# Optimization experiments

Hardware: AMD Instinct MI355X
Metric: run time of the kernel (lower is better)

The kernel has to match this reference:

```python
import jax, jax.numpy as jnp
import numpy as np

N_HEADS = 16
D_MODEL = 1024
D_K = D_MODEL // N_HEADS


def setup_inputs() -> dict:
    key = jax.random.key(0)
    ks = jax.random.split(key, 7)
    B, S = 2, 2048
    init = 0.02
    return {
        "query": jax.random.normal(ks[0], (B, S, D_MODEL), dtype=jnp.float32),
        "key": jax.random.normal(ks[1], (B, S, D_MODEL), dtype=jnp.float32),
        "value": jax.random.normal(ks[2], (B, S, D_MODEL), dtype=jnp.float32),
        "W_q": jax.random.normal(ks[3], (D_MODEL, D_MODEL), dtype=jnp.float32) * init,
        "W_k": jax.random.normal(ks[4], (D_MODEL, D_MODEL), dtype=jnp.float32) * init,
        "W_v": jax.random.normal(ks[5], (D_MODEL, D_MODEL), dtype=jnp.float32) * init,
        "W_o": jax.random.normal(ks[6], (D_MODEL, D_MODEL), dtype=jnp.float32) * init,
    }


def _split_heads(x):
    # (B, S, d_model) -> (B, H, S, d_k)
    B, S, _ = x.shape
    return x.reshape(B, S, N_HEADS, D_K).transpose(0, 2, 1, 3)


def reference(query, key, value, W_q, W_k, W_v, W_o):
    scale = jnp.sqrt(jnp.asarray(D_K, dtype=query.dtype))
    # torch Linear: y = x @ W.T
    Q = _split_heads(query @ W_q.T)   # (B,H,Sq,dk)
    K = _split_heads(key @ W_k.T)     # (B,H,Sk,dk)
    V = _split_heads(value @ W_v.T)   # (B,H,Sk,dk)
    scores = jnp.einsum("bhqd,bhkd->bhqk", Q, K) / scale
    attn = jax.nn.softmax(scores, axis=-1)           # (B,H,Sq,Sk); dropout p=0 -> identity
    attn_weights = attn.mean(axis=1)                 # (B,Sq,Sk) interpretable weights
    head_out = jnp.einsum("bhqk,bhkd->bqhd", attn, V)  # (B,Sq,H,dk)
    # NOTE: the original computes a head-gating (W_h) whose result is overwritten
    # by the concat below -> dead code, omitted.
    B, Sq = head_out.shape[0], head_out.shape[1]
    out = head_out.reshape(B, Sq, D_MODEL) @ W_o.T   # (B,Sq,d_model)
    return (out, attn_weights)
```

## Files before the change

### kernel.cpp

```cpp
#include <hip/hip_runtime.h>
#include <hip/hip_bf16.h>

#define Bq 2
#define Hh 16
#define Ss 2048
#define Dm 1024
#define Dk 64
#define SCALE 0.125f

typedef _Float16 f16x8 __attribute__((ext_vector_type(8)));
typedef _Float16 f16x4 __attribute__((ext_vector_type(4)));
typedef float    f32x4 __attribute__((ext_vector_type(4)));


__device__ __forceinline__ void gl_lds16(const void* g, void* lds) {
    __builtin_amdgcn_global_load_lds(
        (const __attribute__((address_space(1))) void*)g,
        (__attribute__((address_space(3))) void*)lds, 16, 0, 0);
}

__global__ __launch_bounds__(256) void convert_kernel(
    const float* __restrict__ q, const float* __restrict__ k,
    const float* __restrict__ v, const float* __restrict__ wq,
    const float* __restrict__ wk, const float* __restrict__ wv,
    const float* __restrict__ wo,
    _Float16* __restrict__ qd, _Float16* __restrict__ kd,
    _Float16* __restrict__ vd, _Float16* __restrict__ wd)
{
    int seg = blockIdx.y;
    const float* src; _Float16* dst; int n4;
    switch (seg) {
        case 0: src = q; dst = qd; n4 = 1048576; break;
        case 1: src = k; dst = kd; n4 = 1048576; break;
        case 2: src = v; dst = vd; n4 = 1048576; break;
        default:
            src = (seg == 3) ? wq : (seg == 4) ? wk : (seg == 5) ? wv : wo;
            dst = wd + (size_t)(seg - 3) * 1048576;
            n4 = 262144;
    }
    for (int i = blockIdx.x * 256 + threadIdx.x; i < n4; i += gridDim.x * 256) {
        float4 x = ((const float4*)src)[i];
        f16x4 h = {(_Float16)x.x, (_Float16)x.y, (_Float16)x.z, (_Float16)x.w};
        ((f16x4*)dst)[i] = h;
    }
}

__global__ __launch_bounds__(256) void gemm_qkv(
    const _Float16* __restrict__ qf, const _Float16* __restrict__ kf,
    const _Float16* __restrict__ vf, const _Float16* __restrict__ Wh,
    _Float16* __restrict__ Qd, _Float16* __restrict__ Kd,
    _Float16* __restrict__ Vd)
{
    __shared__ _Float16 As[128 * 32];
    __shared__ _Float16 Ws[128 * 32];
    int z = blockIdx.z;
    const _Float16* A = (z == 0) ? qf : (z == 1) ? kf : vf;
    const _Float16* W = Wh + (size_t)z * (Dm * Dm);
    int t = threadIdx.x, lane = t & 63, w = t >> 6;
    int quad = lane >> 4, l15 = lane & 15;
    int wm = w & 1, wn = w >> 1;
    int n0 = blockIdx.x * 128, m0 = blockIdx.y * 128;

    f32x4 acc[4][4] = {};
    for (int k0 = 0; k0 < Dm; k0 += 32) {
        __syncthreads();
        for (int j = 0; j < 2; ++j) {
            int ca = w * 128 + j * 64 + lane;
            int row = ca >> 2, c8 = (ca & 3) * 8;
            gl_lds16(&A[(size_t)(m0 + row) * Dm + k0 + c8],
                     &As[(size_t)(w * 128 + j * 64) * 8]);
            gl_lds16(&W[(size_t)(n0 + row) * Dm + k0 + c8],
                     &Ws[(size_t)(w * 128 + j * 64) * 8]);
        }
        __syncthreads();
        f16x8 af[4], bf[4];
        for (int mi = 0; mi < 4; ++mi)
            af[mi] = *(const f16x8*)&As[(wm * 64 + mi * 16 + l15) * 32 + quad * 8];
        for (int ni = 0; ni < 4; ++ni)
            bf[ni] = *(const f16x8*)&Ws[(wn * 64 + ni * 16 + l15) * 32 + quad * 8];
        for (int mi = 0; mi < 4; ++mi)
            for (int ni = 0; ni < 4; ++ni)
                acc[mi][ni] = __builtin_amdgcn_mfma_f32_16x16x32_f16(
                    af[mi], bf[ni], acc[mi][ni], 0, 0, 0);
    }
    _Float16* Y = (z == 0) ? Qd : (z == 1) ? Kd : Vd;
    for (int mi = 0; mi < 4; ++mi)
        for (int ni = 0; ni < 4; ++ni)
            for (int r = 0; r < 4; ++r) {
                int m = m0 + wm * 64 + mi * 16 + quad * 4 + r;
                int n = n0 + wn * 64 + ni * 16 + l15;
                int b = m >> 11, s = m & (Ss - 1);
                int h = n >> 6,  d = n & 63;
                _Float16 v = (_Float16)acc[mi][ni][r];
                if (z < 2)
                    Y[(((size_t)(b * Hh + h) * Ss + s) << 6) + d] = v;
                else
                    Y[((size_t)(b * Hh + h) * Dk + d) * Ss + s] = v;
            }
}

__global__ __launch_bounds__(256) void gemm_out(
    const _Float16* __restrict__ HO, const _Float16* __restrict__ Woh,
    float* __restrict__ out)
{
    __shared__ _Float16 As[128 * 32];
    __shared__ _Float16 Ws[64 * 32];
    int t = threadIdx.x, lane = t & 63, w = t >> 6;
    int quad = lane >> 4, l15 = lane & 15;
    int n0 = blockIdx.x * 64, m0 = blockIdx.y * 128;

    f32x4 acc[2][4] = {};
    for (int k0 = 0; k0 < Dm; k0 += 32) {
        __syncthreads();
        for (int j = 0; j < 2; ++j) {
            int ca = w * 128 + j * 64 + lane;
            int row = ca >> 2, c8 = (ca & 3) * 8;
            gl_lds16(&HO[(size_t)(m0 + row) * Dm + k0 + c8],
                     &As[(size_t)(w * 128 + j * 64) * 8]);
        }
        {
            int cw = w * 64 + lane;
            int row = cw >> 2, c8 = (cw & 3) * 8;
            gl_lds16(&Woh[(size_t)(n0 + row) * Dm + k0 + c8],
                     &Ws[(size_t)(w * 64) * 8]);
        }
        __syncthreads();
        f16x8 af[2], bf[4];
        for (int mi = 0; mi < 2; ++mi)
            af[mi] = *(const f16x8*)&As[(w * 32 + mi * 16 + l15) * 32 + quad * 8];
        for (int ni = 0; ni < 4; ++ni)
            bf[ni] = *(const f16x8*)&Ws[(ni * 16 + l15) * 32 + quad * 8];
        for (int mi = 0; mi < 2; ++mi)
            for (int ni = 0; ni < 4; ++ni)
                acc[mi][ni] = __builtin_amdgcn_mfma_f32_16x16x32_f16(
                    af[mi], bf[ni], acc[mi][ni], 0, 0, 0);
    }
    for (int mi = 0; mi < 2; ++mi)
        for (int ni = 0; ni < 4; ++ni)
            for (int r = 0; r < 4; ++r) {
                int m = m0 + w * 32 + mi * 16 + quad * 4 + r;
                int n = n0 + ni * 16 + l15;
                out[(size_t)m * Dm + n] = acc[mi][ni][r];
            }
}

__global__ __launch_bounds__(256) void flash_kernel(
    const _Float16* __restrict__ Qh, const _Float16* __restrict__ Kh,
    const _Float16* __restrict__ Vt, _Float16* __restrict__ HO,
    float* __restrict__ lw)
{
    __shared__ alignas(16) _Float16 Ks[64][72];
    __shared__ alignas(16) _Float16 Vs[64][72];
    __shared__ alignas(16) _Float16 Ps[4][32][72];
    int t = threadIdx.x;
    int lane = t & 63, w = t >> 6;
    int quad = lane >> 4, l15 = lane & 15;
    int bh = blockIdx.x;
    int q0 = blockIdx.y * 128 + w * 32;

    const _Float16* Qp = Qh + (size_t)bh * Ss * Dk;
    const _Float16* Kp = Kh + (size_t)bh * Ss * Dk;
    const _Float16* Vp = Vt + (size_t)bh * Dk * Ss;

    f16x8 qf[2][2];
    for (int qh = 0; qh < 2; ++qh)
        for (int kf = 0; kf < 2; ++kf)
            qf[qh][kf] = *(const f16x8*)
                &Qp[(size_t)(q0 + qh * 16 + l15) * Dk + kf * 32 + quad * 8];

    f32x4 o_acc[2][4] = {};
    float lsum[2] = {0.f, 0.f};

    for (int kt = 0; kt < Ss / 64; ++kt) {
        __syncthreads();
        for (int i = 0; i < 2; ++i) {
            int e = i * 256 + t; int row = e >> 3, col = (e & 7) * 8;
            *(f16x8*)&Ks[row][col] =
                *(const f16x8*)&Kp[(size_t)(kt * 64 + row) * Dk + col];
            *(f16x8*)&Vs[row][col] =
                *(const f16x8*)&Vp[(size_t)row * Ss + kt * 64 + col];
        }
        __syncthreads();

        for (int nt = 0; nt < 4; ++nt) {
            f16x8 kf0 = *(const f16x8*)&Ks[nt * 16 + l15][quad * 8];
            f16x8 kf1 = *(const f16x8*)&Ks[nt * 16 + l15][32 + quad * 8];
            for (int qh = 0; qh < 2; ++qh) {
                f32x4 z = {};
                z = __builtin_amdgcn_mfma_f32_16x16x32_f16(kf0, qf[qh][0], z, 0, 0, 0);
                z = __builtin_amdgcn_mfma_f32_16x16x32_f16(kf1, qf[qh][1], z, 0, 0, 0);
                float p0 = __expf(z[0] * SCALE);
                float p1 = __expf(z[1] * SCALE);
                float p2 = __expf(z[2] * SCALE);
                float p3 = __expf(z[3] * SCALE);
                lsum[qh] += (p0 + p1) + (p2 + p3);
                f16x4 hv = {(_Float16)p0, (_Float16)p1, (_Float16)p2, (_Float16)p3};
                *(f16x4*)&Ps[w][qh * 16 + l15][nt * 16 + quad * 4] = hv;
            }
        }

        f16x8 vf[4][2];
        for (int dt = 0; dt < 4; ++dt) {
            vf[dt][0] = *(const f16x8*)&Vs[dt * 16 + l15][quad * 8];
            vf[dt][1] = *(const f16x8*)&Vs[dt * 16 + l15][32 + quad * 8];
        }
        for (int qh = 0; qh < 2; ++qh) {
            f16x8 pf0 = *(const f16x8*)&Ps[w][qh * 16 + l15][quad * 8];
            f16x8 pf1 = *(const f16x8*)&Ps[w][qh * 16 + l15][32 + quad * 8];
            for (int dt = 0; dt < 4; ++dt) {
                o_acc[qh][dt] = __builtin_amdgcn_mfma_f32_16x16x32_f16(
                    pf0, vf[dt][0], o_acc[qh][dt], 0, 0, 0);
                o_acc[qh][dt] = __builtin_amdgcn_mfma_f32_16x16x32_f16(
                    pf1, vf[dt][1], o_acc[qh][dt], 0, 0, 0);
            }
        }
    }

    for (int qh = 0; qh < 2; ++qh) {
        lsum[qh] += __shfl_xor(lsum[qh], 16);
        lsum[qh] += __shfl_xor(lsum[qh], 32);
    }

    int b = bh >> 4, h = bh & 15;
    for (int qh = 0; qh < 2; ++qh) {
        float ir[4];
        for (int r = 0; r < 4; ++r)
            ir[r] = 1.0f / __shfl(lsum[qh], quad * 4 + r);
        for (int dt = 0; dt < 4; ++dt)
            for (int r = 0; r < 4; ++r) {
                int q = q0 + qh * 16 + quad * 4 + r;
                HO[((size_t)(b * Ss + q)) * Dm + h * Dk + dt * 16 + l15] =
                    (_Float16)(o_acc[qh][dt][r] * ir[r]);
            }
        if (lane < 16)
            lw[(size_t)bh * Ss + q0 + qh * 16 + lane] = lsum[qh];
    }
}

__global__ __launch_bounds__(256) void attn_mean_kernel(
    const _Float16* __restrict__ Qh, const _Float16* __restrict__ Kh,
    const float* __restrict__ lw, float* __restrict__ out_attn)
{
    __shared__ alignas(16) _Float16 Ks[64][72];
    int t = threadIdx.x;
    int lane = t & 63, w = t >> 6;
    int quad = lane >> 4, l15 = lane & 15;
    int k0 = blockIdx.x * 64;
    int q0 = blockIdx.y * 64;
    int b  = blockIdx.z;
    int qrow = q0 + w * 16;

    int srow0 = t >> 3, scol0 = (t & 7) * 8;
    int srow1 = (256 + t) >> 3, scol1 = scol0;

    f16x8 kr0, kr1, qn0, qn1;
    float4 ln;
    {
        size_t base = (size_t)(b * Hh) * Ss;
        kr0 = *(const f16x8*)&Kh[(base + k0 + srow0) * Dk + scol0];
        kr1 = *(const f16x8*)&Kh[(base + k0 + srow1) * Dk + scol1];
        qn0 = *(const f16x8*)&Qh[(base + qrow + l15) * Dk + quad * 8];
        qn1 = *(const f16x8*)&Qh[(base + qrow + l15) * Dk + 32 + quad * 8];
        ln  = *(const float4*)&lw[base + qrow + quad * 4];
    }

    f32x4 acc[4] = {};
    for (int h = 0; h < Hh; ++h) {
        __syncthreads();
        *(f16x8*)&Ks[srow0][scol0] = kr0;
        *(f16x8*)&Ks[srow1][scol1] = kr1;
        f16x8 qf0 = qn0, qf1 = qn1;
        float4 lv = ln;
        if (h < Hh - 1) {
            size_t base = (size_t)(b * Hh + h + 1) * Ss;
            kr0 = *(const f16x8*)&Kh[(base + k0 + srow0) * Dk + scol0];
            kr1 = *(const f16x8*)&Kh[(base + k0 + srow1) * Dk + scol1];
            qn0 = *(const f16x8*)&Qh[(base + qrow + l15) * Dk + quad * 8];
            qn1 = *(const f16x8*)&Qh[(base + qrow + l15) * Dk + 32 + quad * 8];
            ln  = *(const float4*)&lw[base + qrow + quad * 4];
        }
        __syncthreads();

        float ir[4] = {1.0f / lv.x, 1.0f / lv.y, 1.0f / lv.z, 1.0f / lv.w};
        for (int nt = 0; nt < 4; ++nt) {
            f16x8 b0 = *(const f16x8*)&Ks[nt * 16 + l15][quad * 8];
            f16x8 b1 = *(const f16x8*)&Ks[nt * 16 + l15][32 + quad * 8];
            f32x4 z = {};
            z = __builtin_amdgcn_mfma_f32_16x16x32_f16(qf0, b0, z, 0, 0, 0);
            z = __builtin_amdgcn_mfma_f32_16x16x32_f16(qf1, b1, z, 0, 0, 0);
            for (int r = 0; r < 4; ++r)
                acc[nt][r] += __expf(z[r] * SCALE) * ir[r];
        }
    }

    for (int nt = 0; nt < 4; ++nt)
        for (int r = 0; r < 4; ++r) {
            int q = qrow + quad * 4 + r;
            out_attn[((size_t)(b * Ss + q)) * Ss + k0 + nt * 16 + l15] =
                acc[nt][r] * (1.0f / Hh);
        }
}

extern "C" void kernel_launch(void* const* d_in, const int* in_sizes, int n_in,
                              void* d_out, int out_size, void* d_ws, size_t ws_size,
                              hipStream_t stream) {
    const float* query = (const float*)d_in[0];
    const float* key   = (const float*)d_in[1];
    const float* value = (const float*)d_in[2];
    const float* Wq    = (const float*)d_in[3];
    const float* Wk    = (const float*)d_in[4];
    const float* Wv    = (const float*)d_in[5];
    const float* Wo    = (const float*)d_in[6];

    float* out      = (float*)d_out;
    float* attn_out = out + (size_t)4194304;

    _Float16* HO = (_Float16*)attn_out;
    _Float16* qf = (_Float16*)(attn_out + 2097152);
    _Float16* kf = qf + 4194304;
    _Float16* vf = kf + 4194304;

    _Float16* Qh = (_Float16*)d_ws;
    _Float16* Kh = Qh + (size_t)4194304;
    _Float16* Vt = Kh + (size_t)4194304;
    _Float16* Wh = Vt + (size_t)4194304;
    float*    lw = (float*)(Wh + (size_t)4194304);

    convert_kernel<<<dim3(256, 7), 256, 0, stream>>>(
        query, key, value, Wq, Wk, Wv, Wo, qf, kf, vf, Wh);

    gemm_qkv<<<dim3(8, 32, 3), 256, 0, stream>>>(qf, kf, vf, Wh, Qh, Kh, Vt);

    flash_kernel<<<dim3(Bq * Hh, Ss / 128), 256, 0, stream>>>(Qh, Kh, Vt, HO, lw);

    gemm_out<<<dim3(16, 32), 256, 0, stream>>>(HO, Wh + (size_t)3 * 1048576, out);

    attn_mean_kernel<<<dim3(Ss / 64, Ss / 64, Bq), 256, 0, stream>>>(
        Qh, Kh, lw, attn_out);
}
```

Before: 308.7 us.

## Split flash attention over key range, add reduce kernel, widen attn-mean tiles

The flash kernel now splits the key sequence into two halves along a new grid dimension, which doubles the block count. Each half writes unnormalized fp16 partial outputs and row sums, and a new reduce kernel combines them and normalizes into the head-output layout. K/V tile loads are register-prefetched one iteration ahead. The attention-mean kernel processes 32 query rows per warp instead of 16, reusing each LDS K tile across two query halves and halving its grid. The changes add an extra launch, partial-buffer traffic through scratch space in the output buffer, and fp16 rounding of unnormalized partial sums.

```diff
diff --git a/kernel.cpp b/kernel.cpp
--- a/kernel.cpp
+++ b/kernel.cpp
@@ -146,8 +146,8 @@
 
 __global__ __launch_bounds__(256) void flash_kernel(
     const _Float16* __restrict__ Qh, const _Float16* __restrict__ Kh,
-    const _Float16* __restrict__ Vt, _Float16* __restrict__ HO,
-    float* __restrict__ lw)
+    const _Float16* __restrict__ Vt, _Float16* __restrict__ Op,
+    float* __restrict__ lp)
 {
     __shared__ alignas(16) _Float16 Ks[64][72];
     __shared__ alignas(16) _Float16 Vs[64][72];
@@ -157,6 +157,8 @@
     int quad = lane >> 4, l15 = lane & 15;
     int bh = blockIdx.x;
     int q0 = blockIdx.y * 128 + w * 32;
+    int ks = blockIdx.z;
+    int kt0 = ks * 16, kt1 = kt0 + 16;
 
     const _Float16* Qp = Qh + (size_t)bh * Ss * Dk;
     const _Float16* Kp = Kh + (size_t)bh * Ss * Dk;
@@ -168,17 +170,28 @@
             qf[qh][kf] = *(const f16x8*)
                 &Qp[(size_t)(q0 + qh * 16 + l15) * Dk + kf * 32 + quad * 8];
 
+    int row0 = t >> 3,         col0 = (t & 7) * 8;
+    int row1 = (256 + t) >> 3, col1 = col0;
+
+    f16x8 kr0 = *(const f16x8*)&Kp[(size_t)(kt0 * 64 + row0) * Dk + col0];
+    f16x8 kr1 = *(const f16x8*)&Kp[(size_t)(kt0 * 64 + row1) * Dk + col1];
+    f16x8 vr0 = *(const f16x8*)&Vp[(size_t)row0 * Ss + kt0 * 64 + col0];
+    f16x8 vr1 = *(const f16x8*)&Vp[(size_t)row1 * Ss + kt0 * 64 + col1];
+
     f32x4 o_acc[2][4] = {};
     float lsum[2] = {0.f, 0.f};
 
-    for (int kt = 0; kt < Ss / 64; ++kt) {
-        __syncthreads();
-        for (int i = 0; i < 2; ++i) {
-            int e = i * 256 + t; int row = e >> 3, col = (e & 7) * 8;
-            *(f16x8*)&Ks[row][col] =
-                *(const f16x8*)&Kp[(size_t)(kt * 64 + row) * Dk + col];
-            *(f16x8*)&Vs[row][col] =
-                *(const f16x8*)&Vp[(size_t)row * Ss + kt * 64 + col];
+    for (int kt = kt0; kt < kt1; ++kt) {
+        __syncthreads();
+        *(f16x8*)&Ks[row0][col0] = kr0;
+        *(f16x8*)&Ks[row1][col1] = kr1;
+        *(f16x8*)&Vs[row0][col0] = vr0;
+        *(f16x8*)&Vs[row1][col1] = vr1;
+        if (kt + 1 < kt1) {
+            kr0 = *(const f16x8*)&Kp[(size_t)((kt + 1) * 64 + row0) * Dk + col0];
+            kr1 = *(const f16x8*)&Kp[(size_t)((kt + 1) * 64 + row1) * Dk + col1];
+            vr0 = *(const f16x8*)&Vp[(size_t)row0 * Ss + (kt + 1) * 64 + col0];
+            vr1 = *(const f16x8*)&Vp[(size_t)row1 * Ss + (kt + 1) * 64 + col1];
         }
         __syncthreads();
 
@@ -221,20 +234,36 @@
         lsum[qh] += __shfl_xor(lsum[qh], 32);
     }
 
-    int b = bh >> 4, h = bh & 15;
+    _Float16* Od = Op + (size_t)ks * (Bq * Hh * Ss * Dk) + (size_t)bh * Ss * Dk;
     for (int qh = 0; qh < 2; ++qh) {
-        float ir[4];
-        for (int r = 0; r < 4; ++r)
-            ir[r] = 1.0f / __shfl(lsum[qh], quad * 4 + r);
         for (int dt = 0; dt < 4; ++dt)
             for (int r = 0; r < 4; ++r) {
                 int q = q0 + qh * 16 + quad * 4 + r;
-                HO[((size_t)(b * Ss + q)) * Dm + h * Dk + dt * 16 + l15] =
-                    (_Float16)(o_acc[qh][dt][r] * ir[r]);
+                Od[(size_t)q * Dk + dt * 16 + l15] = (_Float16)o_acc[qh][dt][r];
             }
         if (lane < 16)
-            lw[(size_t)bh * Ss + q0 + qh * 16 + lane] = lsum[qh];
-    }
+            lp[(size_t)ks * 65536 + (size_t)bh * Ss + q0 + qh * 16 + lane] = lsum[qh];
+    }
+}
+
+__global__ __launch_bounds__(256) void reduce_kernel(
+    const _Float16* __restrict__ Op, const float* __restrict__ lp,
+    _Float16* __restrict__ HO, float* __restrict__ lw)
+{
+    int i = blockIdx.x * 256 + threadIdx.x;
+    int d4  = i & 15;
+    int row = i >> 4;
+    f16x4 a = ((const f16x4*)Op)[i];
+    f16x4 b = ((const f16x4*)Op)[i + 1048576];
+    float l = lp[row] + lp[65536 + row];
+    float inv = 1.0f / l;
+    int bh = row >> 11, q = row & (Ss - 1);
+    int b_ = bh >> 4,  h = bh & 15;
+    f16x4 o;
+    for (int j = 0; j < 4; ++j)
+        o[j] = (_Float16)(((float)a[j] + (float)b[j]) * inv);
+    *(f16x4*)&HO[((size_t)(b_ * Ss + q)) * Dm + h * Dk + d4 * 4] = o;
+    if (d4 == 0) lw[row] = l;
 }
 
 __global__ __launch_bounds__(256) void attn_mean_kernel(
@@ -246,59 +275,73 @@
     int lane = t & 63, w = t >> 6;
     int quad = lane >> 4, l15 = lane & 15;
     int k0 = blockIdx.x * 64;
-    int q0 = blockIdx.y * 64;
+    int q0 = blockIdx.y * 128;
     int b  = blockIdx.z;
-    int qrow = q0 + w * 16;
+    int qrow = q0 + w * 32;
 
     int srow0 = t >> 3, scol0 = (t & 7) * 8;
     int srow1 = (256 + t) >> 3, scol1 = scol0;
 
-    f16x8 kr0, kr1, qn0, qn1;
-    float4 ln;
+    f16x8 kr0, kr1, qn[2][2];
+    float4 ln[2];
     {
         size_t base = (size_t)(b * Hh) * Ss;
         kr0 = *(const f16x8*)&Kh[(base + k0 + srow0) * Dk + scol0];
         kr1 = *(const f16x8*)&Kh[(base + k0 + srow1) * Dk + scol1];
-        qn0 = *(const f16x8*)&Qh[(base + qrow + l15) * Dk + quad * 8];
-        qn1 = *(const f16x8*)&Qh[(base + qrow + l15) * Dk + 32 + quad * 8];
-        ln  = *(const float4*)&lw[base + qrow + quad * 4];
-    }
-
-    f32x4 acc[4] = {};
+        for (int qh = 0; qh < 2; ++qh) {
+            qn[qh][0] = *(const f16x8*)&Qh[(base + qrow + qh * 16 + l15) * Dk + quad * 8];
+            qn[qh][1] = *(const f16x8*)&Qh[(base + qrow + qh * 16 + l15) * Dk + 32 + quad * 8];
+            ln[qh] = *(const float4*)&lw[base + qrow + qh * 16 + quad * 4];
+        }
+    }
+
+    f32x4 acc[2][4] = {};
     for (int h = 0; h < Hh; ++h) {
         __syncthreads();
         *(f16x8*)&Ks[srow0][scol0] = kr0;
         *(f16x8*)&Ks[srow1][scol1] = kr1;
-        f16x8 qf0 = qn0, qf1 = qn1;
-        float4 lv = ln;
+        f16x8 qf[2][2];
+        float4 lv[2];
+        for (int qh = 0; qh < 2; ++qh) {
+            qf[qh][0] = qn[qh][0]; qf[qh][1] = qn[qh][1]; lv[qh] = ln[qh];
+        }
         if (h < Hh - 1) {
             size_t base = (size_t)(b * Hh + h + 1) * Ss;
             kr0 = *(const f16x8*)&Kh[(base + k0 + srow0) * Dk + scol0];
             kr1 = *(const f16x8*)&Kh[(base + k0 + srow1) * Dk + scol1];
-            qn0 = *(const f16x8*)&Qh[(base + qrow + l15) * Dk + quad * 8];
-            qn1 = *(const f16x8*)&Qh[(base + qrow + l15) * Dk + 32 + quad * 8];
-            ln  = *(const float4*)&lw[base + qrow + quad * 4];
-        }
-        __syncthreads();
-
-        float ir[4] = {1.0f / lv.x, 1.0f / lv.y, 1.0f / lv.z, 1.0f / lv.w};
+            for (int qh = 0; qh < 2; ++qh) {
+                qn[qh][0] = *(const f16x8*)&Qh[(base + qrow + qh * 16 + l15) * Dk + quad * 8];
+                qn[qh][1] = *(const f16x8*)&Qh[(base + qrow + qh * 16 + l15) * Dk + 32 + quad * 8];
+                ln[qh] = *(const float4*)&lw[base + qrow + qh * 16 + quad * 4];
+            }
+        }
+        __syncthreads();
+
+        float ir[2][4];
+        for (int qh = 0; qh < 2; ++qh) {
+            ir[qh][0] = 1.0f / lv[qh].x; ir[qh][1] = 1.0f / lv[qh].y;
+            ir[qh][2] = 1.0f / lv[qh].z; ir[qh][3] = 1.0f / lv[qh].w;
+        }
         for (int nt = 0; nt < 4; ++nt) {
             f16x8 b0 = *(const f16x8*)&Ks[nt * 16 + l15][quad * 8];
             f16x8 b1 = *(const f16x8*)&Ks[nt * 16 + l15][32 + quad * 8];
-            f32x4 z = {};
-            z = __builtin_amdgcn_mfma_f32_16x16x32_f16(qf0, b0, z, 0, 0, 0);
-            z = __builtin_amdgcn_mfma_f32_16x16x32_f16(qf1, b1, z, 0, 0, 0);
-            for (int r = 0; r < 4; ++r)
-                acc[nt][r] += __expf(z[r] * SCALE) * ir[r];
-        }
-    }
-
-    for (int nt = 0; nt < 4; ++nt)
-        for (int r = 0; r < 4; ++r) {
-            int q = qrow + quad * 4 + r;
-            out_attn[((size_t)(b * Ss + q)) * Ss + k0 + nt * 16 + l15] =
-                acc[nt][r] * (1.0f / Hh);
-        }
+            for (int qh = 0; qh < 2; ++qh) {
+                f32x4 z = {};
+                z = __builtin_amdgcn_mfma_f32_16x16x32_f16(qf[qh][0], b0, z, 0, 0, 0);
+                z = __builtin_amdgcn_mfma_f32_16x16x32_f16(qf[qh][1], b1, z, 0, 0, 0);
+                for (int r = 0; r < 4; ++r)
+                    acc[qh][nt][r] += __expf(z[r] * SCALE) * ir[qh][r];
+            }
+        }
+    }
+
+    for (int qh = 0; qh < 2; ++qh)
+        for (int nt = 0; nt < 4; ++nt)
+            for (int r = 0; r < 4; ++r) {
+                int q = qrow + qh * 16 + quad * 4 + r;
+                out_attn[((size_t)(b * Ss + q)) * Ss + k0 + nt * 16 + l15] =
+                    acc[qh][nt][r] * (1.0f / Hh);
+            }
 }
 
 extern "C" void kernel_launch(void* const* d_in, const int* in_sizes, int n_in,
@@ -315,10 +358,12 @@
     float* out      = (float*)d_out;
     float* attn_out = out + (size_t)4194304;
 
-    _Float16* HO = (_Float16*)attn_out;
-    _Float16* qf = (_Float16*)(attn_out + 2097152);
-    _Float16* kf = qf + 4194304;
-    _Float16* vf = kf + 4194304;
+    _Float16* HO  = (_Float16*)attn_out;
+    _Float16* qf  = (_Float16*)(attn_out + 2097152);
+    _Float16* kf  = qf + 4194304;
+    _Float16* vf  = kf + 4194304;
+    _Float16* Op  = qf;
+    float*    lp  = (float*)(Op + 2 * 4194304);
 
     _Float16* Qh = (_Float16*)d_ws;
     _Float16* Kh = Qh + (size_t)4194304;
@@ -331,10 +376,12 @@
 
     gemm_qkv<<<dim3(8, 32, 3), 256, 0, stream>>>(qf, kf, vf, Wh, Qh, Kh, Vt);
 
-    flash_kernel<<<dim3(Bq * Hh, Ss / 128), 256, 0, stream>>>(Qh, Kh, Vt, HO, lw);
+    flash_kernel<<<dim3(Bq * Hh, Ss / 128, 2), 256, 0, stream>>>(Qh, Kh, Vt, Op, lp);
+
+    reduce_kernel<<<4096, 256, 0, stream>>>(Op, lp, HO, lw);
 
     gemm_out<<<dim3(16, 32), 256, 0, stream>>>(HO, Wh + (size_t)3 * 1048576, out);
 
-    attn_mean_kernel<<<dim3(Ss / 64, Ss / 64, Bq), 256, 0, stream>>>(
+    attn_mean_kernel<<<dim3(Ss / 64, Ss / 128, Bq), 256, 0, stream>>>(
         Qh, Kh, lw, attn_out);
 }
```

Result: faster. 288.1 us (-6.7%).
